# Kernel tuning notes

Hardware: AMD Instinct MI355X
Metric: run time of the kernel (lower is better)

## Reference

```python
import jax, jax.numpy as jnp
import numpy as np

HEADS = 16


def bemm(x, weight, bias, er, es):
    # BatchEnsembleMM.forward: x [T,B,Hin], weight [Hout,Hin], er [B,Hin], es [B,Hout]
    x_r = x * er[None, :, :]
    x_mm = jnp.einsum('tbh,oh->tbo', x_r, weight)
    return x_mm * es[None, :, :] + bias


def rel_shift(x):
    # RelativeShift.forward (batch_first): x [N, len_q, len_r]
    n, q, r = x.shape
    x_pad = jnp.pad(x, ((0, 0), (0, 0), (1, 0)))        # [N, q, r+1]
    x_view = x_pad.reshape(n, r + 1, q)[:, 1:, :]        # drop first 'row'
    return x_view.reshape(n, q, r)


def setup_inputs() -> dict:
    key = jax.random.key(0)
    ks = jax.random.split(key, 14)
    T, B, H = 1024, 8, 1024
    Lr = 1024
    s = 0.02
    return {
        'inputs': jax.random.normal(ks[0], (T, B, H), jnp.float32),
        'pos': jax.random.normal(ks[1], (Lr, 1, H), jnp.float32),
        'input_weights': jax.random.normal(ks[2], (3 * H, H), jnp.float32) * s,
        'input_biases': jax.random.normal(ks[3], (3 * H,), jnp.float32) * s,
        'pos_weights': jax.random.normal(ks[4], (H, H), jnp.float32) * s,
        'pos_biases': jax.random.normal(ks[5], (H,), jnp.float32) * s,
        'output_weights': jax.random.normal(ks[6], (H, H), jnp.float32) * s,
        'output_biases': jax.random.normal(ks[7], (H,), jnp.float32) * s,
        'r_i': 1.0 + jax.random.normal(ks[8], (B, H), jnp.float32) * 0.1,
        's_i': 1.0 + jax.random.normal(ks[9], (B, 3 * H), jnp.float32) * 0.1,
        'r_p': 1.0 + jax.random.normal(ks[10], (B, H), jnp.float32) * 0.1,
        's_p': 1.0 + jax.random.normal(ks[11], (B, H), jnp.float32) * 0.1,
        'r_w_bias': jax.random.normal(ks[12], (HEADS, H // HEADS), jnp.float32) * s,
        'r_r_bias': jax.random.normal(ks[13], (HEADS, H // HEADS), jnp.float32) * s,
        'heads': HEADS,
    }


def reference(inputs, pos, input_weights, input_biases, pos_weights, pos_biases,
              output_weights, output_biases, r_i, s_i, r_p, s_p,
              r_w_bias, r_r_bias, heads):
    T, B, H = inputs.shape
    hd = H // heads
    scale = hd ** (-0.5)
    Lr = pos.shape[0]

    pos_rep = jnp.broadcast_to(pos, (Lr, B, H))

    # BatchEnsemble QKV and positional projections (training path)
    qkv = bemm(inputs, input_weights, input_biases, r_i, s_i)       # [T,B,3H]
    qkv = qkv.reshape(T, B * heads, 3, hd)
    queries, keys, values = qkv[:, :, 0, :], qkv[:, :, 1, :], qkv[:, :, 2, :]

    r_head_k = bemm(pos_rep, pos_weights, pos_biases, r_p, s_p)     # [Lr,B,H]
    r_head_k = r_head_k.reshape(Lr, B * heads, hd)

    rw_head_q = (queries.reshape(T, B, heads, hd) + r_w_bias).reshape(T, B * heads, hd)
    rr_head_q = (queries.reshape(T, B, heads, hd) + r_r_bias).reshape(T, B * heads, hd)

    # content score AC and position score BD
    matmul_ac = jnp.einsum('qnd,knd->nqk', rw_head_q, keys) * scale    # [B*h,T,T]
    matmul_bd = jnp.einsum('qnd,rnd->nqr', rr_head_q, r_head_k) * scale
    matmul_bd = rel_shift(matmul_bd)[:, :, :T]

    attn_score = matmul_ac + matmul_bd
    softmax_results = jax.nn.softmax(attn_score.astype(jnp.float32), axis=-1).astype(inputs.dtype)

    context = jnp.einsum('nqk,knd->qnd', softmax_results, values).reshape(T, B, H)
    outputs = jnp.einsum('tbh,oh->tbo', context, output_weights) + output_biases
    return outputs
```

## Files before the change

kernel.cpp:

```cpp
#include <hip/hip_runtime.h>
#include <cstdint>
#include <cstddef>

using u16 = unsigned short;
typedef short short8 __attribute__((ext_vector_type(8)));
typedef unsigned short us8 __attribute__((ext_vector_type(8)));
typedef unsigned short us4 __attribute__((ext_vector_type(4)));
typedef float f32x4 __attribute__((ext_vector_type(4)));
typedef float f4 __attribute__((ext_vector_type(4)));

#define T_ 1024
#define B_ 8
#define H_ 1024
#define HEADS_ 16
#define HD_ 64
#define N3_ 3072

__device__ __forceinline__ float b2f(u16 u){
  union { float f; unsigned int i; } v; v.i = ((unsigned int)u) << 16; return v.f;
}
__device__ __forceinline__ u16 f2b(float f){
  union { float f; unsigned int i; } v; v.f = f;
  return (u16)((v.i + 0x8000u) >> 16);
}

template<bool HAS_S, bool SCALE_A, bool POS_A, bool A_BF16, bool OUT_F32>
__global__ __launch_bounds__(256) void k_gemm(const void* __restrict__ A_, const float* __restrict__ W,
                                              const float* __restrict__ RA, const float* __restrict__ S,
                                              const float* __restrict__ bias, void* __restrict__ C_, int N){
  const int K = 1024;
  const int n0 = blockIdx.x * 128, m0 = blockIdx.y * 128;
  const int tid = threadIdx.x, lane = tid & 63;
  const int wave = tid >> 6, wr = wave >> 1, wc = wave & 1;
  __shared__ alignas(16) u16 At[128 * 32];
  __shared__ alignas(16) u16 Bt[128 * 32];
  f32x4 acc[4][4] = {};

  for (int kt = 0; kt < 32; ++kt){
    const int k0 = kt * 32;
    f4 wv[4];
    us8 avb[2];
    f4 avf[4];
#pragma unroll
    for (int i = 0; i < 4; ++i){
      int c = tid + i * 256, r = c >> 3, sg = c & 7;
      wv[i] = *(const f4*)(W + (size_t)(n0 + r) * K + k0 + sg * 4);
    }
    if (A_BF16){
      const u16* A = (const u16*)A_;
#pragma unroll
      for (int i = 0; i < 2; ++i){
        int c = tid + i * 256, r = c >> 2, sg = c & 3;
        avb[i] = *(const us8*)(A + (size_t)(m0 + r) * K + k0 + sg * 8);
      }
    } else {
      const float* A = (const float*)A_;
#pragma unroll
      for (int i = 0; i < 4; ++i){
        int c = tid + i * 256, r = c >> 3, sg = c & 7;
        int m = m0 + r;
        const float* ap = POS_A ? (A + (size_t)(m >> 3) * K + k0 + sg * 4)
                                : (A + (size_t)m * K + k0 + sg * 4);
        avf[i] = *(const f4*)ap;
        if (SCALE_A){
          f4 rv = *(const f4*)(RA + (m & 7) * K + k0 + sg * 4);
          avf[i] = avf[i] * rv;
        }
      }
    }
    __syncthreads();
#pragma unroll
    for (int i = 0; i < 4; ++i){
      int c = tid + i * 256, r = c >> 3, sg = c & 7;
      us4 pw;
#pragma unroll
      for (int u = 0; u < 4; ++u) pw[u] = f2b(wv[i][u]);
      *(us4*)(Bt + r * 32 + sg * 4) = pw;
    }
    if (A_BF16){
#pragma unroll
      for (int i = 0; i < 2; ++i){
        int c = tid + i * 256, r = c >> 2, sg = c & 3;
        *(us8*)(At + r * 32 + sg * 8) = avb[i];
      }
    } else {
#pragma unroll
      for (int i = 0; i < 4; ++i){
        int c = tid + i * 256, r = c >> 3, sg = c & 7;
        us4 pa;
#pragma unroll
        for (int u = 0; u < 4; ++u) pa[u] = f2b(avf[i][u]);
        *(us4*)(At + r * 32 + sg * 4) = pa;
      }
    }
    __syncthreads();
    short8 af[4], bf[4];
#pragma unroll
    for (int i = 0; i < 4; ++i){
      int ar = wr * 64 + i * 16 + (lane & 15);
      af[i] = *(const short8*)(At + ar * 32 + ((lane >> 4) << 3));
      int br = wc * 64 + i * 16 + (lane & 15);
      bf[i] = *(const short8*)(Bt + br * 32 + ((lane >> 4) << 3));
    }
#pragma unroll
    for (int i = 0; i < 4; ++i)
#pragma unroll
      for (int j = 0; j < 4; ++j)
        acc[i][j] = __builtin_amdgcn_mfma_f32_16x16x32_bf16(af[i], bf[j], acc[i][j], 0, 0, 0);
  }
#pragma unroll
  for (int i = 0; i < 4; ++i){
    int row0 = wr * 64 + i * 16 + ((lane >> 4) << 2);
#pragma unroll
    for (int j = 0; j < 4; ++j){
      int o = n0 + wc * 64 + j * 16 + (lane & 15);
      float bv = bias[o];
#pragma unroll
      for (int jj = 0; jj < 4; ++jj){
        int m = m0 + row0 + jj;
        float v = acc[i][j][jj];
        if (HAS_S) v *= S[(m & 7) * N + o];
        v += bv;
        if (OUT_F32) ((float*)C_)[(size_t)m * N + o] = v;
        else         ((u16*)C_)[(size_t)m * N + o] = f2b(v);
      }
    }
  }
}

__global__ __launch_bounds__(256) void k_vt(const u16* __restrict__ qkv, u16* __restrict__ VT){
  const int tt = blockIdx.x;
  const int n = blockIdx.y;
  const int b = n >> 4, head = n & 15;
  __shared__ alignas(16) u16 tile[64][72];
  const int tid = threadIdx.x;
#pragma unroll
  for (int i = 0; i < 2; ++i){
    int c = tid + i * 256;
    int r = c >> 3, sg = c & 7;
    const u16* src = qkv + ((size_t)(tt * 64 + r) * 8 + b) * N3_ + head * 192 + 128 + sg * 8;
    *(us8*)&tile[r][sg * 8] = *(const us8*)src;
  }
  __syncthreads();
#pragma unroll
  for (int i = 0; i < 2; ++i){
    int c = tid + i * 256;
    int d = c >> 3, sg = c & 7;
    us8 ov;
#pragma unroll
    for (int u = 0; u < 8; ++u) ov[u] = tile[sg * 8 + u][d];
    *(us8*)(VT + ((size_t)n * 64 + d) * 1024 + tt * 64 + sg * 8) = ov;
  }
}

#define G_OFF   0
#define RWQ_OFF 67664
#define RRQ_OFF 71760
#define RED_OFF 77904
#define SMEM_SZ 79952

__device__ __forceinline__ int gswz(int byt){ return byt ^ (((byt >> 13) & 3) << 5); }

__global__ __launch_bounds__(512, 2) void k_attn(const u16* __restrict__ qkv, const u16* __restrict__ rk,
                                                 const u16* __restrict__ VTg, const float* __restrict__ rwb,
                                                 const float* __restrict__ rrb, u16* __restrict__ ctx){
  const int bid = blockIdx.x;
  const int n = (bid & 7) + ((bid >> 8) << 3);
  const int qb = (bid >> 3) & 31;
  const int q0 = qb * 32;
  const int bat = n >> 4, head = n & 15;
  const int tid = threadIdx.x, lane = tid & 63, wave = tid >> 6;
  const int l15 = lane & 15, grp = lane >> 4;

  __shared__ alignas(16) char smem[SMEM_SZ];
  char* gB  = smem + G_OFF;
  u16* rwq = (u16*)(smem + RWQ_OFF);
  u16* rrq = (u16*)(smem + RRQ_OFF);
  float* redf = (float*)(smem + RED_OFF);

  const float PRESCALE = 0.125f * 1.44269504089f;
#pragma unroll
  for (int rep = 0; rep < 2; ++rep){
    int c = tid + rep * 512;
    if (c < 640){
      int s = c >> 3, sg = c & 7;
      u16* dst; int row; const float* bias;
      if (s < 32){ dst = rwq; row = s; bias = rwb; }
      else       { dst = rrq; row = s - 32; bias = rrb; }
      int qrow = q0 + row;
      float v[8];
      const float* bp2 = bias + head * 64 + sg * 8;
      if (qrow < T_){
        const u16* qp = qkv + ((size_t)qrow * 8 + bat) * N3_ + head * 192 + sg * 8;
        us8 qv = *(const us8*)qp;
        f4 b0 = *(const f4*)bp2, b1 = *(const f4*)(bp2 + 4);
#pragma unroll
        for (int u = 0; u < 4; ++u){
          v[u]     = (b2f(qv[u])     + b0[u]) * PRESCALE;
          v[u + 4] = (b2f(qv[u + 4]) + b1[u]) * PRESCALE;
        }
      } else {
#pragma unroll
        for (int u = 0; u < 8; ++u) v[u] = 0.f;
      }
      us8 pk;
#pragma unroll
      for (int u = 0; u < 8; ++u) pk[u] = f2b(v[u]);
      *(us8*)((char*)dst + row * 128 + ((sg * 16) ^ ((row & 7) << 4))) = pk;
    }
  }
  if (tid < 33) *(u16*)(gB + gswz(tid * 2050 + 2048)) = 0;

  auto ldf = [&](const void* base, int row, int kkb)->short8 {
    int co = kkb + (grp << 4);
    return *(const short8*)((const char*)base + row * 128 + (co ^ ((row & 7) << 4)));
  };

  __syncthreads();

#pragma unroll
  for (int s = 0; s < 2; ++s){
    short8 af[3][2];
#pragma unroll
    for (int pi = 0; pi < 3; ++pi)
#pragma unroll
      for (int kk = 0; kk < 2; ++kk) af[pi][kk] = ldf(rrq, pi * 16 + l15, kk * 64);
#pragma unroll
    for (int c4 = 0; c4 < 4; ++c4){
      int r = s * 512 + wave * 64 + c4 * 16 + l15;
      const u16* bp = rk + ((size_t)r * 8 + bat) * 1024 + head * 64 + grp * 8;
      short8 bf0 = *(const short8*)bp;
      short8 bf1 = *(const short8*)(bp + 32);
      int rg = s * 512 + wave * 64 + c4 * 16 + l15;
#pragma unroll
      for (int pi = 0; pi < 3; ++pi){
        f32x4 acc = {0.f, 0.f, 0.f, 0.f};
        acc = __builtin_amdgcn_mfma_f32_16x16x32_bf16(af[pi][0], bf0, acc, 0, 0, 0);
        acc = __builtin_amdgcn_mfma_f32_16x16x32_bf16(af[pi][1], bf1, acc, 0, 0, 0);
#pragma unroll
        for (int jj = 0; jj < 4; ++jj){
          int a = pi * 16 + (grp << 2) + jj;
          if (a < 33) *(u16*)(gB + gswz(a * 2050 + (rg << 1))) = f2b(acc[jj]);
        }
      }
    }
  }
  __syncthreads();

  f32x4 p[2][2][4];
  float pm[2][4];
#pragma unroll
  for (int m = 0; m < 2; ++m)
#pragma unroll
    for (int jj = 0; jj < 4; ++jj) pm[m][jj] = -3.0e38f;

#pragma unroll
  for (int s = 0; s < 2; ++s){
    short8 af[2][2];
#pragma unroll
    for (int m = 0; m < 2; ++m)
#pragma unroll
      for (int kk = 0; kk < 2; ++kk) af[m][kk] = ldf(rwq, m * 16 + l15, kk * 64);
#pragma unroll
    for (int c4 = 0; c4 < 4; ++c4){
      int bcol = s * 512 + wave * 64 + c4 * 16 + l15;
      const u16* kp = qkv + ((size_t)bcol * 8 + bat) * N3_ + head * 192 + 64 + grp * 8;
      short8 bf0 = *(const short8*)kp;
      short8 bf1 = *(const short8*)(kp + 32);
      int byt0 = ((1023 - q0 + bcol) << 1) + (grp << 13);
#pragma unroll
      for (int m = 0; m < 2; ++m){
        f32x4 acc = {0.f, 0.f, 0.f, 0.f};
        acc = __builtin_amdgcn_mfma_f32_16x16x32_bf16(af[m][0], bf0, acc, 0, 0, 0);
        acc = __builtin_amdgcn_mfma_f32_16x16x32_bf16(af[m][1], bf1, acc, 0, 0, 0);
#pragma unroll
        for (int jj = 0; jj < 4; ++jj){
          int byt = byt0 + (m << 15) + (jj << 11);
          float gv = b2f(*(const u16*)(gB + gswz(byt)));
          float sc = acc[jj] + gv;
          p[s][m][c4][jj] = sc;
          pm[m][jj] = fmaxf(pm[m][jj], sc);
        }
      }
    }
  }

#pragma unroll
  for (int m = 0; m < 2; ++m)
#pragma unroll
    for (int jj = 0; jj < 4; ++jj)
#pragma unroll
      for (int mk = 1; mk < 16; mk <<= 1) pm[m][jj] = fmaxf(pm[m][jj], __shfl_xor(pm[m][jj], mk));
  if (l15 == 0){
#pragma unroll
    for (int m = 0; m < 2; ++m)
#pragma unroll
      for (int jj = 0; jj < 4; ++jj) redf[wave * 32 + m * 16 + (grp << 2) + jj] = pm[m][jj];
  }
  __syncthreads();
  float M_[2][4];
#pragma unroll
  for (int m = 0; m < 2; ++m)
#pragma unroll
    for (int jj = 0; jj < 4; ++jj){
      int row = m * 16 + (grp << 2) + jj;
      float v = redf[row];
#pragma unroll
      for (int w = 1; w < 8; ++w) v = fmaxf(v, redf[w * 32 + row]);
      M_[m][jj] = v;
    }

  char* ptW = smem + G_OFF + wave * 8192;
  float L_[2][4] = {};
#pragma unroll
  for (int s = 0; s < 2; ++s)
#pragma unroll
    for (int m = 0; m < 2; ++m)
#pragma unroll
      for (int c4 = 0; c4 < 4; ++c4)
#pragma unroll
        for (int jj = 0; jj < 4; ++jj){
          float e = __builtin_exp2f(p[s][m][c4][jj] - M_[m][jj]);
          L_[m][jj] += e;
          int q = m * 16 + (grp << 2) + jj;
          int tl = s * 64 + c4 * 16 + l15;
          *(u16*)(ptW + q * 256 + ((tl * 2) ^ ((q & 7) << 4))) = f2b(e);
        }
#pragma unroll
  for (int m = 0; m < 2; ++m)
#pragma unroll
    for (int jj = 0; jj < 4; ++jj)
#pragma unroll
      for (int mk = 1; mk < 16; mk <<= 1) L_[m][jj] += __shfl_xor(L_[m][jj], mk);
  if (l15 == 0){
#pragma unroll
    for (int m = 0; m < 2; ++m)
#pragma unroll
      for (int jj = 0; jj < 4; ++jj) redf[256 + wave * 32 + m * 16 + (grp << 2) + jj] = L_[m][jj];
  }
  __syncthreads();

  f32x4 Oacc[2][4] = {};
#pragma unroll
  for (int s = 0; s < 2; ++s){
#pragma unroll
    for (int kk = 0; kk < 2; ++kk){
      short8 pa[2];
#pragma unroll
      for (int m = 0; m < 2; ++m)
        pa[m] = *(const short8*)(ptW + (m * 16 + l15) * 256 + ((s * 128 + kk * 64 + (grp << 4)) ^ ((l15 & 7) << 4)));
      int tg = s * 512 + wave * 64 + kk * 32 + grp * 8;
#pragma unroll
      for (int dt = 0; dt < 4; ++dt){
        int dr = dt * 16 + l15;
        short8 vb = *(const short8*)(VTg + ((size_t)n * 64 + dr) * 1024 + tg);
#pragma unroll
        for (int m = 0; m < 2; ++m)
          Oacc[m][dt] = __builtin_amdgcn_mfma_f32_16x16x32_bf16(pa[m], vb, Oacc[m][dt], 0, 0, 0);
      }
    }
  }

  float* par = (float*)ptW;
#pragma unroll
  for (int m = 0; m < 2; ++m)
#pragma unroll
    for (int dt = 0; dt < 4; ++dt)
#pragma unroll
      for (int jj = 0; jj < 4; ++jj)
        par[(m * 16 + (grp << 2) + jj) * 64 + dt * 16 + l15] = Oacc[m][dt][jj];
  __syncthreads();
  {
    float* parAll = (float*)(smem + G_OFF);
    f32x4 v = {0.f, 0.f, 0.f, 0.f};
#pragma unroll
    for (int w = 0; w < 8; ++w) v += *(const f32x4*)(parAll + w * 2048 + tid * 4);
    int q = tid >> 4, d4 = (tid & 15) * 4;
    float sum = 0.f;
#pragma unroll
    for (int w = 0; w < 8; ++w) sum += redf[256 + w * 32 + q];
    float il = 1.0f / (sum + 1e-20f);
    us4 pk;
#pragma unroll
    for (int e = 0; e < 4; ++e) pk[e] = f2b(v[e] * il);
    *(us4*)(ctx + ((size_t)(q0 + q) * 8 + bat) * 1024 + head * 64 + d4) = pk;
  }
}

extern "C" void kernel_launch(void* const* d_in, const int* in_sizes, int n_in,
                              void* d_out, int out_size, void* d_ws, size_t ws_size,
                              hipStream_t stream){
  const float* x   = (const float*)d_in[0];
  const float* pos = (const float*)d_in[1];
  const float* Wi  = (const float*)d_in[2];
  const float* bi  = (const float*)d_in[3];
  const float* Wp  = (const float*)d_in[4];
  const float* bp  = (const float*)d_in[5];
  const float* Wo  = (const float*)d_in[6];
  const float* bo  = (const float*)d_in[7];
  const float* r_i = (const float*)d_in[8];
  const float* s_i = (const float*)d_in[9];
  const float* r_p = (const float*)d_in[10];
  const float* s_p = (const float*)d_in[11];
  const float* rwb = (const float*)d_in[12];
  const float* rrb = (const float*)d_in[13];

  const size_t MB = 1024 * 1024;
  u16* qkv = (u16*)((char*)d_ws);
  u16* rk  = (u16*)((char*)d_ws + 48 * MB);
  u16* VTg  = (u16*)d_out;
  u16* ctxg = (u16*)((char*)d_out + 16777216);

  k_gemm<true,  true,  false, false, false><<<dim3(24, 64), 256, 0, stream>>>(x,   Wi, r_i, s_i, bi, qkv, N3_);
  k_gemm<true,  true,  true,  false, false><<<dim3(8, 64),  256, 0, stream>>>(pos, Wp, r_p, s_p, bp, rk, 1024);
  k_vt<<<dim3(16, 128), 256, 0, stream>>>(qkv, VTg);
  k_attn<<<dim3(4096), 512, 0, stream>>>(qkv, rk, VTg, rwb, rrb, ctxg);
  hipMemcpyAsync(qkv, ctxg, (size_t)out_size * sizeof(u16), hipMemcpyDeviceToDevice, stream);
  k_gemm<false, false, false, true, true><<<dim3(8, 64), 256, 0, stream>>>(qkv, Wo, nullptr, nullptr, bo, (float*)d_out, 1024);
}
```

Baseline: 481.7 us.

## Halve attention query tile to 16 rows to raise occupancy

The attention kernel now handles 16 query rows per block instead of 32, doubling the grid to 8192 blocks. Shared memory per block roughly halves, per-thread accumulator and score registers halve, and the launch hint now asks for 4 waves per EU to fit more blocks per CU. The cost is that each block reloads the full K, V and positional-key streams for half as many queries, doubling that global/L2 traffic. Each block also computes half as many positional-score rows, so the extra shifted row it needs is a larger share of its work.

Result: slower. 565.4 us (+17.4%).

```diff
diff --git a/kernel.cpp b/kernel.cpp
--- a/kernel.cpp
+++ b/kernel.cpp
@@ -6,6 +6,7 @@
 typedef short short8 __attribute__((ext_vector_type(8)));
 typedef unsigned short us8 __attribute__((ext_vector_type(8)));
 typedef unsigned short us4 __attribute__((ext_vector_type(4)));
+typedef unsigned short us2 __attribute__((ext_vector_type(2)));
 typedef float f32x4 __attribute__((ext_vector_type(4)));
 typedef float f4 __attribute__((ext_vector_type(4)));
 
@@ -154,20 +155,21 @@
 }
 
 #define G_OFF   0
-#define RWQ_OFF 67664
-#define RRQ_OFF 71760
-#define RED_OFF 77904
-#define SMEM_SZ 79952
+#define RWQ_OFF 34880
+#define RRQ_OFF 36928
+#define RED_OFF 41024
+#define SMEM_SZ 42048
 
 __device__ __forceinline__ int gswz(int byt){ return byt ^ (((byt >> 13) & 3) << 5); }
 
-__global__ __launch_bounds__(512, 2) void k_attn(const u16* __restrict__ qkv, const u16* __restrict__ rk,
-                                                 const u16* __restrict__ VTg, const float* __restrict__ rwb,
-                                                 const float* __restrict__ rrb, u16* __restrict__ ctx){
+__global__ __launch_bounds__(512) __attribute__((amdgpu_waves_per_eu(4)))
+void k_attn(const u16* __restrict__ qkv, const u16* __restrict__ rk,
+            const u16* __restrict__ VTg, const float* __restrict__ rwb,
+            const float* __restrict__ rrb, u16* __restrict__ ctx){
   const int bid = blockIdx.x;
-  const int n = (bid & 7) + ((bid >> 8) << 3);
-  const int qb = (bid >> 3) & 31;
-  const int q0 = qb * 32;
+  const int n = (bid & 7) + ((bid >> 9) << 3);
+  const int qb = (bid >> 3) & 63;
+  const int q0 = qb * 16;
   const int bat = n >> 4, head = n & 15;
   const int tid = threadIdx.x, lane = tid & 63, wave = tid >> 6;
   const int l15 = lane & 15, grp = lane >> 4;
@@ -179,14 +181,13 @@
   float* redf = (float*)(smem + RED_OFF);
 
   const float PRESCALE = 0.125f * 1.44269504089f;
-#pragma unroll
-  for (int rep = 0; rep < 2; ++rep){
-    int c = tid + rep * 512;
-    if (c < 640){
+  {
+    int c = tid;
+    if (c < 384){
       int s = c >> 3, sg = c & 7;
       u16* dst; int row; const float* bias;
-      if (s < 32){ dst = rwq; row = s; bias = rwb; }
-      else       { dst = rrq; row = s - 32; bias = rrb; }
+      if (s < 16){ dst = rwq; row = s; bias = rwb; }
+      else       { dst = rrq; row = s - 16; bias = rrb; }
       int qrow = q0 + row;
       float v[8];
       const float* bp2 = bias + head * 64 + sg * 8;
@@ -209,7 +210,7 @@
       *(us8*)((char*)dst + row * 128 + ((sg * 16) ^ ((row & 7) << 4))) = pk;
     }
   }
-  if (tid < 33) *(u16*)(gB + gswz(tid * 2050 + 2048)) = 0;
+  if (tid < 17) *(u16*)(gB + gswz(tid * 2050 + 2048)) = 0;
 
   auto ldf = [&](const void* base, int row, int kkb)->short8 {
     int co = kkb + (grp << 4);
@@ -218,172 +219,145 @@
 
   __syncthreads();
 
-#pragma unroll
-  for (int s = 0; s < 2; ++s){
-    short8 af[3][2];
-#pragma unroll
-    for (int pi = 0; pi < 3; ++pi)
+  {
+    short8 af[2][2];
+#pragma unroll
+    for (int pi = 0; pi < 2; ++pi)
 #pragma unroll
       for (int kk = 0; kk < 2; ++kk) af[pi][kk] = ldf(rrq, pi * 16 + l15, kk * 64);
 #pragma unroll
-    for (int c4 = 0; c4 < 4; ++c4){
-      int r = s * 512 + wave * 64 + c4 * 16 + l15;
-      const u16* bp = rk + ((size_t)r * 8 + bat) * 1024 + head * 64 + grp * 8;
-      short8 bf0 = *(const short8*)bp;
-      short8 bf1 = *(const short8*)(bp + 32);
-      int rg = s * 512 + wave * 64 + c4 * 16 + l15;
-#pragma unroll
-      for (int pi = 0; pi < 3; ++pi){
+    for (int s = 0; s < 2; ++s){
+#pragma unroll
+      for (int c4 = 0; c4 < 4; ++c4){
+        int r = s * 512 + wave * 64 + c4 * 16 + l15;
+        const u16* bp = rk + ((size_t)r * 8 + bat) * 1024 + head * 64 + grp * 8;
+        short8 bf0 = *(const short8*)bp;
+        short8 bf1 = *(const short8*)(bp + 32);
+#pragma unroll
+        for (int pi = 0; pi < 2; ++pi){
+          f32x4 acc = {0.f, 0.f, 0.f, 0.f};
+          acc = __builtin_amdgcn_mfma_f32_16x16x32_bf16(af[pi][0], bf0, acc, 0, 0, 0);
+          acc = __builtin_amdgcn_mfma_f32_16x16x32_bf16(af[pi][1], bf1, acc, 0, 0, 0);
+#pragma unroll
+          for (int jj = 0; jj < 4; ++jj){
+            int a = pi * 16 + (grp << 2) + jj;
+            if (a < 17) *(u16*)(gB + gswz(a * 2050 + (r << 1))) = f2b(acc[jj]);
+          }
+        }
+      }
+    }
+  }
+  __syncthreads();
+
+  f32x4 p[2][4];
+  float pm[4] = {-3.0e38f, -3.0e38f, -3.0e38f, -3.0e38f};
+  {
+    short8 af[2];
+#pragma unroll
+    for (int kk = 0; kk < 2; ++kk) af[kk] = ldf(rwq, l15, kk * 64);
+#pragma unroll
+    for (int s = 0; s < 2; ++s){
+#pragma unroll
+      for (int c4 = 0; c4 < 4; ++c4){
+        int bcol = s * 512 + wave * 64 + c4 * 16 + l15;
+        const u16* kp = qkv + ((size_t)bcol * 8 + bat) * N3_ + head * 192 + 64 + grp * 8;
+        short8 bf0 = *(const short8*)kp;
+        short8 bf1 = *(const short8*)(kp + 32);
         f32x4 acc = {0.f, 0.f, 0.f, 0.f};
-        acc = __builtin_amdgcn_mfma_f32_16x16x32_bf16(af[pi][0], bf0, acc, 0, 0, 0);
-        acc = __builtin_amdgcn_mfma_f32_16x16x32_bf16(af[pi][1], bf1, acc, 0, 0, 0);
+        acc = __builtin_amdgcn_mfma_f32_16x16x32_bf16(af[0], bf0, acc, 0, 0, 0);
+        acc = __builtin_amdgcn_mfma_f32_16x16x32_bf16(af[1], bf1, acc, 0, 0, 0);
+        int byt0 = ((1023 - q0 + bcol) << 1) + (grp << 13);
 #pragma unroll
         for (int jj = 0; jj < 4; ++jj){
-          int a = pi * 16 + (grp << 2) + jj;
-          if (a < 33) *(u16*)(gB + gswz(a * 2050 + (rg << 1))) = f2b(acc[jj]);
-        }
-      }
-    }
-  }
-  __syncthreads();
-
-  f32x4 p[2][2][4];
-  float pm[2][4];
-#pragma unroll
-  for (int m = 0; m < 2; ++m)
-#pragma unroll
-    for (int jj = 0; jj < 4; ++jj) pm[m][jj] = -3.0e38f;
-
-#pragma unroll
-  for (int s = 0; s < 2; ++s){
-    short8 af[2][2];
-#pragma unroll
-    for (int m = 0; m < 2; ++m)
-#pragma unroll
-      for (int kk = 0; kk < 2; ++kk) af[m][kk] = ldf(rwq, m * 16 + l15, kk * 64);
-#pragma unroll
-    for (int c4 = 0; c4 < 4; ++c4){
-      int bcol = s * 512 + wave * 64 + c4 * 16 + l15;
-      const u16* kp = qkv + ((size_t)bcol * 8 + bat) * N3_ + head * 192 + 64 + grp * 8;
-      short8 bf0 = *(const short8*)kp;
-      short8 bf1 = *(const short8*)(kp + 32);
-      int byt0 = ((1023 - q0 + bcol) << 1) + (grp << 13);
-#pragma unroll
-      for (int m = 0; m < 2; ++m){
-        f32x4 acc = {0.f, 0.f, 0.f, 0.f};
-        acc = __builtin_amdgcn_mfma_f32_16x16x32_bf16(af[m][0], bf0, acc, 0, 0, 0);
-        acc = __builtin_amdgcn_mfma_f32_16x16x32_bf16(af[m][1], bf1, acc, 0, 0, 0);
-#pragma unroll
-        for (int jj = 0; jj < 4; ++jj){
-          int byt = byt0 + (m << 15) + (jj << 11);
+          int byt = byt0 + (jj << 11);
           float gv = b2f(*(const u16*)(gB + gswz(byt)));
           float sc = acc[jj] + gv;
-          p[s][m][c4][jj] = sc;
-          pm[m][jj] = fmaxf(pm[m][jj], sc);
+          p[s][c4][jj] = sc;
+          pm[jj] = fmaxf(pm[jj], sc);
         }
       }
     }
   }
 
 #pragma unroll
-  for (int m = 0; m < 2; ++m)
-#pragma unroll
-    for (int jj = 0; jj < 4; ++jj)
-#pragma unroll
-      for (int mk = 1; mk < 16; mk <<= 1) pm[m][jj] = fmaxf(pm[m][jj], __shfl_xor(pm[m][jj], mk));
+  for (int jj = 0; jj < 4; ++jj)
+#pragma unroll
+    for (int mk = 1; mk < 16; mk <<= 1) pm[jj] = fmaxf(pm[jj], __shfl_xor(pm[jj], mk));
   if (l15 == 0){
 #pragma unroll
-    for (int m = 0; m < 2; ++m)
-#pragma unroll
-      for (int jj = 0; jj < 4; ++jj) redf[wave * 32 + m * 16 + (grp << 2) + jj] = pm[m][jj];
-  }
-  __syncthreads();
-  float M_[2][4];
-#pragma unroll
-  for (int m = 0; m < 2; ++m)
-#pragma unroll
-    for (int jj = 0; jj < 4; ++jj){
-      int row = m * 16 + (grp << 2) + jj;
-      float v = redf[row];
-#pragma unroll
-      for (int w = 1; w < 8; ++w) v = fmaxf(v, redf[w * 32 + row]);
-      M_[m][jj] = v;
-    }
-
-  char* ptW = smem + G_OFF + wave * 8192;
-  float L_[2][4] = {};
+    for (int jj = 0; jj < 4; ++jj) redf[wave * 16 + (grp << 2) + jj] = pm[jj];
+  }
+  __syncthreads();
+  float M_[4];
+#pragma unroll
+  for (int jj = 0; jj < 4; ++jj){
+    int row = (grp << 2) + jj;
+    float v = redf[row];
+#pragma unroll
+    for (int w = 1; w < 8; ++w) v = fmaxf(v, redf[w * 16 + row]);
+    M_[jj] = v;
+  }
+
+  char* ptW = smem + G_OFF + wave * 4096;
+  float L_[4] = {};
 #pragma unroll
   for (int s = 0; s < 2; ++s)
 #pragma unroll
-    for (int m = 0; m < 2; ++m)
-#pragma unroll
-      for (int c4 = 0; c4 < 4; ++c4)
-#pragma unroll
-        for (int jj = 0; jj < 4; ++jj){
-          float e = __builtin_exp2f(p[s][m][c4][jj] - M_[m][jj]);
-          L_[m][jj] += e;
-          int q = m * 16 + (grp << 2) + jj;
-          int tl = s * 64 + c4 * 16 + l15;
-          *(u16*)(ptW + q * 256 + ((tl * 2) ^ ((q & 7) << 4))) = f2b(e);
-        }
-#pragma unroll
-  for (int m = 0; m < 2; ++m)
-#pragma unroll
-    for (int jj = 0; jj < 4; ++jj)
-#pragma unroll
-      for (int mk = 1; mk < 16; mk <<= 1) L_[m][jj] += __shfl_xor(L_[m][jj], mk);
+    for (int c4 = 0; c4 < 4; ++c4)
+#pragma unroll
+      for (int jj = 0; jj < 4; ++jj){
+        float e = __builtin_exp2f(p[s][c4][jj] - M_[jj]);
+        L_[jj] += e;
+        int q = (grp << 2) + jj;
+        int tl = s * 64 + c4 * 16 + l15;
+        *(u16*)(ptW + q * 256 + ((tl * 2) ^ ((q & 7) << 4))) = f2b(e);
+      }
+#pragma unroll
+  for (int jj = 0; jj < 4; ++jj)
+#pragma unroll
+    for (int mk = 1; mk < 16; mk <<= 1) L_[jj] += __shfl_xor(L_[jj], mk);
   if (l15 == 0){
 #pragma unroll
-    for (int m = 0; m < 2; ++m)
-#pragma unroll
-      for (int jj = 0; jj < 4; ++jj) redf[256 + wave * 32 + m * 16 + (grp << 2) + jj] = L_[m][jj];
-  }
-  __syncthreads();
-
-  f32x4 Oacc[2][4] = {};
+    for (int jj = 0; jj < 4; ++jj) redf[128 + wave * 16 + (grp << 2) + jj] = L_[jj];
+  }
+  __syncthreads();
+
+  f32x4 Oacc[4] = {};
 #pragma unroll
   for (int s = 0; s < 2; ++s){
 #pragma unroll
     for (int kk = 0; kk < 2; ++kk){
-      short8 pa[2];
-#pragma unroll
-      for (int m = 0; m < 2; ++m)
-        pa[m] = *(const short8*)(ptW + (m * 16 + l15) * 256 + ((s * 128 + kk * 64 + (grp << 4)) ^ ((l15 & 7) << 4)));
+      short8 pa = *(const short8*)(ptW + l15 * 256 + ((s * 128 + kk * 64 + (grp << 4)) ^ ((l15 & 7) << 4)));
       int tg = s * 512 + wave * 64 + kk * 32 + grp * 8;
 #pragma unroll
       for (int dt = 0; dt < 4; ++dt){
         int dr = dt * 16 + l15;
         short8 vb = *(const short8*)(VTg + ((size_t)n * 64 + dr) * 1024 + tg);
-#pragma unroll
-        for (int m = 0; m < 2; ++m)
-          Oacc[m][dt] = __builtin_amdgcn_mfma_f32_16x16x32_bf16(pa[m], vb, Oacc[m][dt], 0, 0, 0);
+        Oacc[dt] = __builtin_amdgcn_mfma_f32_16x16x32_bf16(pa, vb, Oacc[dt], 0, 0, 0);
       }
     }
   }
 
   float* par = (float*)ptW;
 #pragma unroll
-  for (int m = 0; m < 2; ++m)
-#pragma unroll
-    for (int dt = 0; dt < 4; ++dt)
-#pragma unroll
-      for (int jj = 0; jj < 4; ++jj)
-        par[(m * 16 + (grp << 2) + jj) * 64 + dt * 16 + l15] = Oacc[m][dt][jj];
+  for (int dt = 0; dt < 4; ++dt)
+#pragma unroll
+    for (int jj = 0; jj < 4; ++jj)
+      par[((grp << 2) + jj) * 64 + dt * 16 + l15] = Oacc[dt][jj];
   __syncthreads();
   {
     float* parAll = (float*)(smem + G_OFF);
-    f32x4 v = {0.f, 0.f, 0.f, 0.f};
-#pragma unroll
-    for (int w = 0; w < 8; ++w) v += *(const f32x4*)(parAll + w * 2048 + tid * 4);
-    int q = tid >> 4, d4 = (tid & 15) * 4;
-    float sum = 0.f;
-#pragma unroll
-    for (int w = 0; w < 8; ++w) sum += redf[256 + w * 32 + q];
+    int q = tid >> 5, dp = (tid & 31) * 2;
+    float v0 = 0.f, v1 = 0.f, sum = 0.f;
+#pragma unroll
+    for (int w = 0; w < 8; ++w){
+      const float* pw = parAll + w * 1024 + q * 64 + dp;
+      v0 += pw[0]; v1 += pw[1];
+      sum += redf[128 + w * 16 + q];
+    }
     float il = 1.0f / (sum + 1e-20f);
-    us4 pk;
-#pragma unroll
-    for (int e = 0; e < 4; ++e) pk[e] = f2b(v[e] * il);
-    *(us4*)(ctx + ((size_t)(q0 + q) * 8 + bat) * 1024 + head * 64 + d4) = pk;
+    us2 pk; pk[0] = f2b(v0 * il); pk[1] = f2b(v1 * il);
+    *(us2*)(ctx + ((size_t)(q0 + q) * 8 + bat) * 1024 + head * 64 + dp) = pk;
   }
 }
 
@@ -414,7 +388,7 @@
   k_gemm<true,  true,  false, false, false><<<dim3(24, 64), 256, 0, stream>>>(x,   Wi, r_i, s_i, bi, qkv, N3_);
   k_gemm<true,  true,  true,  false, false><<<dim3(8, 64),  256, 0, stream>>>(pos, Wp, r_p, s_p, bp, rk, 1024);
   k_vt<<<dim3(16, 128), 256, 0, stream>>>(qkv, VTg);
-  k_attn<<<dim3(4096), 512, 0, stream>>>(qkv, rk, VTg, rwb, rrb, ctxg);
+  k_attn<<<dim3(8192), 512, 0, stream>>>(qkv, rk, VTg, rwb, rrb, ctxg);
   hipMemcpyAsync(qkv, ctxg, (size_t)out_size * sizeof(u16), hipMemcpyDeviceToDevice, stream);
   k_gemm<false, false, false, true, true><<<dim3(8, 64), 256, 0, stream>>>(qkv, Wo, nullptr, nullptr, bo, (float*)d_out, 1024);
 }
```

## Use per-wave online softmax with register-resident P and lazy rescaling

Applied to the files above, without the earlier changes.

Replaces the two-pass softmax (block-wide max reduction, then exp and writing P to LDS) with a per-wave online softmax. The QK MFMA is computed transposed, so its probabilities feed the PV MFMA straight from registers. Running maxima are rescaled only when a new max exceeds the old one by more than a threshold, and per-wave partials are merged at the end with exp2 correction factors. This removes a block barrier, the LDS round trip for P, and the large score register array, and it changes the launch hint to waves_per_eu(4) plus the LDS swizzle for the new access pattern. In exchange it adds shuffles, scattered 4-element V loads and a divergent rescale branch.

After: 452.3 us. 6.1% less time.

```diff
diff --git a/kernel.cpp b/kernel.cpp
--- a/kernel.cpp
+++ b/kernel.cpp
@@ -4,6 +4,7 @@
 
 using u16 = unsigned short;
 typedef short short8 __attribute__((ext_vector_type(8)));
+typedef short short4v __attribute__((ext_vector_type(4)));
 typedef unsigned short us8 __attribute__((ext_vector_type(8)));
 typedef unsigned short us4 __attribute__((ext_vector_type(4)));
 typedef float f32x4 __attribute__((ext_vector_type(4)));
@@ -159,11 +160,14 @@
 #define RED_OFF 77904
 #define SMEM_SZ 79952
 
-__device__ __forceinline__ int gswz(int byt){ return byt ^ (((byt >> 13) & 3) << 5); }
-
-__global__ __launch_bounds__(512, 2) void k_attn(const u16* __restrict__ qkv, const u16* __restrict__ rk,
-                                                 const u16* __restrict__ VTg, const float* __restrict__ rwb,
-                                                 const float* __restrict__ rrb, u16* __restrict__ ctx){
+__device__ __forceinline__ int gswz(int byt){
+  return byt ^ (((byt >> 11) & 1) << 2) ^ (((byt >> 13) & 3) << 5);
+}
+
+__global__ __launch_bounds__(512) __attribute__((amdgpu_waves_per_eu(4)))
+void k_attn(const u16* __restrict__ qkv, const u16* __restrict__ rk,
+            const u16* __restrict__ VTg, const float* __restrict__ rwb,
+            const float* __restrict__ rrb, u16* __restrict__ ctx){
   const int bid = blockIdx.x;
   const int n = (bid & 7) + ((bid >> 8) << 3);
   const int qb = (bid >> 3) & 31;
@@ -218,150 +222,136 @@
 
   __syncthreads();
 
-#pragma unroll
-  for (int s = 0; s < 2; ++s){
+  {
     short8 af[3][2];
 #pragma unroll
     for (int pi = 0; pi < 3; ++pi)
 #pragma unroll
       for (int kk = 0; kk < 2; ++kk) af[pi][kk] = ldf(rrq, pi * 16 + l15, kk * 64);
 #pragma unroll
-    for (int c4 = 0; c4 < 4; ++c4){
-      int r = s * 512 + wave * 64 + c4 * 16 + l15;
-      const u16* bp = rk + ((size_t)r * 8 + bat) * 1024 + head * 64 + grp * 8;
-      short8 bf0 = *(const short8*)bp;
-      short8 bf1 = *(const short8*)(bp + 32);
-      int rg = s * 512 + wave * 64 + c4 * 16 + l15;
-#pragma unroll
-      for (int pi = 0; pi < 3; ++pi){
-        f32x4 acc = {0.f, 0.f, 0.f, 0.f};
-        acc = __builtin_amdgcn_mfma_f32_16x16x32_bf16(af[pi][0], bf0, acc, 0, 0, 0);
-        acc = __builtin_amdgcn_mfma_f32_16x16x32_bf16(af[pi][1], bf1, acc, 0, 0, 0);
-#pragma unroll
-        for (int jj = 0; jj < 4; ++jj){
-          int a = pi * 16 + (grp << 2) + jj;
-          if (a < 33) *(u16*)(gB + gswz(a * 2050 + (rg << 1))) = f2b(acc[jj]);
+    for (int s = 0; s < 2; ++s){
+#pragma unroll
+      for (int c4 = 0; c4 < 4; ++c4){
+        int r = s * 512 + wave * 64 + c4 * 16 + l15;
+        const u16* bp = rk + ((size_t)r * 8 + bat) * 1024 + head * 64 + grp * 8;
+        short8 bf0 = *(const short8*)bp;
+        short8 bf1 = *(const short8*)(bp + 32);
+#pragma unroll
+        for (int pi = 0; pi < 3; ++pi){
+          f32x4 acc = {0.f, 0.f, 0.f, 0.f};
+          acc = __builtin_amdgcn_mfma_f32_16x16x32_bf16(af[pi][0], bf0, acc, 0, 0, 0);
+          acc = __builtin_amdgcn_mfma_f32_16x16x32_bf16(af[pi][1], bf1, acc, 0, 0, 0);
+#pragma unroll
+          for (int jj = 0; jj < 4; ++jj){
+            int a = pi * 16 + (grp << 2) + jj;
+            if (a < 33) *(u16*)(gB + gswz(a * 2050 + (r << 1))) = f2b(acc[jj]);
+          }
         }
       }
     }
   }
   __syncthreads();
 
-  f32x4 p[2][2][4];
-  float pm[2][4];
+  short8 qf[2][2];
 #pragma unroll
   for (int m = 0; m < 2; ++m)
 #pragma unroll
-    for (int jj = 0; jj < 4; ++jj) pm[m][jj] = -3.0e38f;
-
-#pragma unroll
-  for (int s = 0; s < 2; ++s){
-    short8 af[2][2];
-#pragma unroll
-    for (int m = 0; m < 2; ++m)
-#pragma unroll
-      for (int kk = 0; kk < 2; ++kk) af[m][kk] = ldf(rwq, m * 16 + l15, kk * 64);
-#pragma unroll
-    for (int c4 = 0; c4 < 4; ++c4){
-      int bcol = s * 512 + wave * 64 + c4 * 16 + l15;
-      const u16* kp = qkv + ((size_t)bcol * 8 + bat) * N3_ + head * 192 + 64 + grp * 8;
-      short8 bf0 = *(const short8*)kp;
-      short8 bf1 = *(const short8*)(kp + 32);
-      int byt0 = ((1023 - q0 + bcol) << 1) + (grp << 13);
+    for (int kk = 0; kk < 2; ++kk) qf[m][kk] = ldf(rwq, m * 16 + l15, kk * 64);
+
+  float m_run[2] = {-3.0e38f, -3.0e38f};
+  float l_run[2] = {0.f, 0.f};
+  f32x4 Oacc[2][4] = {};
+
+#pragma unroll
+  for (int pr = 0; pr < 4; ++pr){
+    int base = wave * 64 + (pr & 1) * 32 + (pr >> 1) * 512;
+    float s_[2][2][4];
+#pragma unroll
+    for (int h = 0; h < 2; ++h){
+      int cb = base + h * 16;
+      const u16* kp = qkv + ((size_t)(cb + l15) * 8 + bat) * N3_ + head * 192 + 64 + grp * 8;
+      short8 kf0 = *(const short8*)kp;
+      short8 kf1 = *(const short8*)(kp + 32);
 #pragma unroll
       for (int m = 0; m < 2; ++m){
         f32x4 acc = {0.f, 0.f, 0.f, 0.f};
-        acc = __builtin_amdgcn_mfma_f32_16x16x32_bf16(af[m][0], bf0, acc, 0, 0, 0);
-        acc = __builtin_amdgcn_mfma_f32_16x16x32_bf16(af[m][1], bf1, acc, 0, 0, 0);
+        acc = __builtin_amdgcn_mfma_f32_16x16x32_bf16(kf0, qf[m][0], acc, 0, 0, 0);
+        acc = __builtin_amdgcn_mfma_f32_16x16x32_bf16(kf1, qf[m][1], acc, 0, 0, 0);
+        int aa = m * 16 + l15;
 #pragma unroll
         for (int jj = 0; jj < 4; ++jj){
-          int byt = byt0 + (m << 15) + (jj << 11);
-          float gv = b2f(*(const u16*)(gB + gswz(byt)));
-          float sc = acc[jj] + gv;
-          p[s][m][c4][jj] = sc;
-          pm[m][jj] = fmaxf(pm[m][jj], sc);
+          int bcol = cb + (grp << 2) + jj;
+          int byt = (aa << 11) + ((1023 - q0 + bcol) << 1);
+          s_[h][m][jj] = acc[jj] + b2f(*(const u16*)(gB + gswz(byt)));
         }
       }
     }
-  }
-
-#pragma unroll
-  for (int m = 0; m < 2; ++m)
-#pragma unroll
-    for (int jj = 0; jj < 4; ++jj)
-#pragma unroll
-      for (int mk = 1; mk < 16; mk <<= 1) pm[m][jj] = fmaxf(pm[m][jj], __shfl_xor(pm[m][jj], mk));
-  if (l15 == 0){
-#pragma unroll
-    for (int m = 0; m < 2; ++m)
-#pragma unroll
-      for (int jj = 0; jj < 4; ++jj) redf[wave * 32 + m * 16 + (grp << 2) + jj] = pm[m][jj];
+    float cm[2];
+#pragma unroll
+    for (int m = 0; m < 2; ++m){
+      float c0 = fmaxf(fmaxf(s_[0][m][0], s_[0][m][1]), fmaxf(s_[0][m][2], s_[0][m][3]));
+      float c1 = fmaxf(fmaxf(s_[1][m][0], s_[1][m][1]), fmaxf(s_[1][m][2], s_[1][m][3]));
+      float c = fmaxf(c0, c1);
+      c = fmaxf(c, __shfl_xor(c, 16));
+      c = fmaxf(c, __shfl_xor(c, 32));
+      cm[m] = c;
+    }
+    if (!__all(cm[0] <= m_run[0] + 8.f && cm[1] <= m_run[1] + 8.f)){
+#pragma unroll
+      for (int m = 0; m < 2; ++m){
+        float mn = fmaxf(m_run[m], cm[m]);
+        float f = __builtin_exp2f(m_run[m] - mn);
+        l_run[m] *= f;
+        m_run[m] = mn;
+#pragma unroll
+        for (int jj = 0; jj < 4; ++jj){
+          float fq = __shfl(f, (lane & 48) + ((lane >> 2) & 12) + jj);
+#pragma unroll
+          for (int dt = 0; dt < 4; ++dt) Oacc[m][dt][jj] *= fq;
+        }
+      }
+    }
+    short8 pa[2];
+#pragma unroll
+    for (int m = 0; m < 2; ++m){
+      float ls = 0.f;
+#pragma unroll
+      for (int jj = 0; jj < 4; ++jj){
+        float e0 = __builtin_exp2f(s_[0][m][jj] - m_run[m]);
+        float e1 = __builtin_exp2f(s_[1][m][jj] - m_run[m]);
+        ls += e0 + e1;
+        pa[m][jj]     = (short)f2b(e0);
+        pa[m][4 + jj] = (short)f2b(e1);
+      }
+      l_run[m] += ls;
+    }
+#pragma unroll
+    for (int dt = 0; dt < 4; ++dt){
+      const u16* vp = VTg + ((size_t)n * 64 + dt * 16 + l15) * 1024 + base + (grp << 2);
+      short4v v0 = *(const short4v*)vp;
+      short4v v1 = *(const short4v*)(vp + 16);
+      short8 vb = {v0[0], v0[1], v0[2], v0[3], v1[0], v1[1], v1[2], v1[3]};
+#pragma unroll
+      for (int m = 0; m < 2; ++m)
+        Oacc[m][dt] = __builtin_amdgcn_mfma_f32_16x16x32_bf16(pa[m], vb, Oacc[m][dt], 0, 0, 0);
+    }
+  }
+
+#pragma unroll
+  for (int m = 0; m < 2; ++m){
+    l_run[m] += __shfl_xor(l_run[m], 16);
+    l_run[m] += __shfl_xor(l_run[m], 32);
+  }
+  if (grp == 0){
+#pragma unroll
+    for (int m = 0; m < 2; ++m){
+      redf[wave * 32 + m * 16 + l15] = m_run[m];
+      redf[256 + wave * 32 + m * 16 + l15] = l_run[m];
+    }
   }
   __syncthreads();
-  float M_[2][4];
-#pragma unroll
-  for (int m = 0; m < 2; ++m)
-#pragma unroll
-    for (int jj = 0; jj < 4; ++jj){
-      int row = m * 16 + (grp << 2) + jj;
-      float v = redf[row];
-#pragma unroll
-      for (int w = 1; w < 8; ++w) v = fmaxf(v, redf[w * 32 + row]);
-      M_[m][jj] = v;
-    }
-
-  char* ptW = smem + G_OFF + wave * 8192;
-  float L_[2][4] = {};
-#pragma unroll
-  for (int s = 0; s < 2; ++s)
-#pragma unroll
-    for (int m = 0; m < 2; ++m)
-#pragma unroll
-      for (int c4 = 0; c4 < 4; ++c4)
-#pragma unroll
-        for (int jj = 0; jj < 4; ++jj){
-          float e = __builtin_exp2f(p[s][m][c4][jj] - M_[m][jj]);
-          L_[m][jj] += e;
-          int q = m * 16 + (grp << 2) + jj;
-          int tl = s * 64 + c4 * 16 + l15;
-          *(u16*)(ptW + q * 256 + ((tl * 2) ^ ((q & 7) << 4))) = f2b(e);
-        }
-#pragma unroll
-  for (int m = 0; m < 2; ++m)
-#pragma unroll
-    for (int jj = 0; jj < 4; ++jj)
-#pragma unroll
-      for (int mk = 1; mk < 16; mk <<= 1) L_[m][jj] += __shfl_xor(L_[m][jj], mk);
-  if (l15 == 0){
-#pragma unroll
-    for (int m = 0; m < 2; ++m)
-#pragma unroll
-      for (int jj = 0; jj < 4; ++jj) redf[256 + wave * 32 + m * 16 + (grp << 2) + jj] = L_[m][jj];
-  }
-  __syncthreads();
-
-  f32x4 Oacc[2][4] = {};
-#pragma unroll
-  for (int s = 0; s < 2; ++s){
-#pragma unroll
-    for (int kk = 0; kk < 2; ++kk){
-      short8 pa[2];
-#pragma unroll
-      for (int m = 0; m < 2; ++m)
-        pa[m] = *(const short8*)(ptW + (m * 16 + l15) * 256 + ((s * 128 + kk * 64 + (grp << 4)) ^ ((l15 & 7) << 4)));
-      int tg = s * 512 + wave * 64 + kk * 32 + grp * 8;
-#pragma unroll
-      for (int dt = 0; dt < 4; ++dt){
-        int dr = dt * 16 + l15;
-        short8 vb = *(const short8*)(VTg + ((size_t)n * 64 + dr) * 1024 + tg);
-#pragma unroll
-        for (int m = 0; m < 2; ++m)
-          Oacc[m][dt] = __builtin_amdgcn_mfma_f32_16x16x32_bf16(pa[m], vb, Oacc[m][dt], 0, 0, 0);
-      }
-    }
-  }
-
-  float* par = (float*)ptW;
+
+  float* par = (float*)(smem + wave * 8192);
 #pragma unroll
   for (int m = 0; m < 2; ++m)
 #pragma unroll
@@ -370,16 +360,23 @@
       for (int jj = 0; jj < 4; ++jj)
         par[(m * 16 + (grp << 2) + jj) * 64 + dt * 16 + l15] = Oacc[m][dt][jj];
   __syncthreads();
+
   {
-    float* parAll = (float*)(smem + G_OFF);
+    float* parAll = (float*)smem;
+    int q = tid >> 4, d4 = (tid & 15) * 4;
+    float M = -3.0e38f;
+#pragma unroll
+    for (int w = 0; w < 8; ++w) M = fmaxf(M, redf[w * 32 + q]);
     f32x4 v = {0.f, 0.f, 0.f, 0.f};
-#pragma unroll
-    for (int w = 0; w < 8; ++w) v += *(const f32x4*)(parAll + w * 2048 + tid * 4);
-    int q = tid >> 4, d4 = (tid & 15) * 4;
-    float sum = 0.f;
-#pragma unroll
-    for (int w = 0; w < 8; ++w) sum += redf[256 + w * 32 + q];
-    float il = 1.0f / (sum + 1e-20f);
+    float L = 0.f;
+#pragma unroll
+    for (int w = 0; w < 8; ++w){
+      float sc = __builtin_exp2f(redf[w * 32 + q] - M);
+      L += redf[256 + w * 32 + q] * sc;
+      f32x4 pv = *(const f32x4*)(parAll + w * 2048 + q * 64 + d4);
+      v += pv * sc;
+    }
+    float il = 1.0f / (L + 1e-20f);
     us4 pk;
 #pragma unroll
     for (int e = 0; e < 4; ++e) pk[e] = f2b(v[e] * il);
```
